# Kernel tuning notes

Measured on AMD Instinct MI355X. Metric: run time of the kernel, lower is better.

## Reference

```python
import jax, jax.numpy as jnp
import numpy as np

N_NODES = 100000
N_EDGES = 1000000
D_IN = 64
D_OUT = 64


def setup_inputs() -> dict:
    key = jax.random.key(0)
    k_feat, k_ei, k_ew, k_w, k_b = jax.random.split(key, 5)
    features = jax.random.normal(k_feat, (N_NODES, D_IN), dtype=jnp.float32)
    edge_index = jax.random.randint(k_ei, (2, N_EDGES), 0, N_NODES, dtype=jnp.int64)
    edge_weight = jax.random.uniform(k_ew, (N_EDGES,), dtype=jnp.float32)
    # nn.Linear(input_dim, output_dim): weight [out, in], bias [out]
    lim = 1.0 / np.sqrt(D_IN)
    W = jax.random.uniform(k_w, (D_OUT, D_IN), minval=-lim, maxval=lim, dtype=jnp.float32)
    b = jax.random.uniform(k_b, (D_OUT,), minval=-lim, maxval=lim, dtype=jnp.float32)
    return {"features": features, "edge_index": edge_index,
            "edge_weight": edge_weight, "W": W, "b": b}


def reference(features, edge_index, edge_weight, W, b):
    # gather source-node features and scale by edge weight: [E, F]
    messages = features[edge_index[0]] * edge_weight[:, None]
    # scatter-add into destination nodes (vectorized form of the per-column
    # scatter_add_ loop in the original): [N, F]
    aggregated = jax.ops.segment_sum(messages, edge_index[1],
                                     num_segments=features.shape[0])
    # residual + linear; dropout is identity in eval mode
    return (aggregated + features) @ W.T + b
```

## Files before the change

kernel.cpp:

```cpp
#include <hip/hip_runtime.h>

constexpr int N_NODES = 100000;
constexpr int N_EDGES = 1000000;
constexpr int D = 64;
constexpr int NTILES = (N_NODES + 1023) / 1024;


__global__ __launch_bounds__(256) void rank_k(
    const int* __restrict__ ei, int* __restrict__ cnt, int* __restrict__ rank)
{
    int e = blockIdx.x * 256 + threadIdx.x;
    if (e >= N_EDGES) return;
    rank[e] = atomicAdd(&cnt[ei[N_EDGES + e]], 1);
}

__global__ __launch_bounds__(256) void hist_k(
    const int* __restrict__ ei, int* __restrict__ hist)
{
    int e = blockIdx.x * 256 + threadIdx.x;
    if (e >= N_EDGES) return;
    atomicAdd(&hist[ei[N_EDGES + e]], 1);
}

__global__ __launch_bounds__(256) void tile_sum_k(
    const int* __restrict__ counts, int* __restrict__ tileSums)
{
    __shared__ int red[256];
    int t = threadIdx.x;
    int base = blockIdx.x * 1024 + t * 4;
    int4 c = make_int4(0, 0, 0, 0);
    if (base + 3 < N_NODES) {
        c = *reinterpret_cast<const int4*>(counts + base);
    } else {
        if (base + 0 < N_NODES) c.x = counts[base + 0];
        if (base + 1 < N_NODES) c.y = counts[base + 1];
        if (base + 2 < N_NODES) c.z = counts[base + 2];
        if (base + 3 < N_NODES) c.w = counts[base + 3];
    }
    red[t] = c.x + c.y + c.z + c.w;
    __syncthreads();
    for (int d = 128; d > 0; d >>= 1) {
        if (t < d) red[t] += red[t + d];
        __syncthreads();
    }
    if (t == 0) tileSums[blockIdx.x] = red[0];
}

__global__ __launch_bounds__(128) void tile_scan_k(
    const int* __restrict__ tileSums, int* __restrict__ tileBase)
{
    __shared__ int s[128];
    int t = threadIdx.x;
    s[t] = (t < NTILES) ? tileSums[t] : 0;
    __syncthreads();
    for (int d = 1; d < 128; d <<= 1) {
        int v = (t >= d) ? s[t - d] : 0;
        __syncthreads();
        s[t] += v;
        __syncthreads();
    }
    if (t < NTILES) tileBase[t] = t ? s[t - 1] : 0;
}

__global__ __launch_bounds__(256) void scan_apply_k(
    int* __restrict__ counts, const int* __restrict__ tileBase,
    int* __restrict__ offsets)
{
    __shared__ int tsum[256];
    int t = threadIdx.x;
    int base = blockIdx.x * 1024 + t * 4;
    int4 c = make_int4(0, 0, 0, 0);
    bool full = (base + 3 < N_NODES);
    if (full) {
        c = *reinterpret_cast<const int4*>(counts + base);
    } else {
        if (base + 0 < N_NODES) c.x = counts[base + 0];
        if (base + 1 < N_NODES) c.y = counts[base + 1];
        if (base + 2 < N_NODES) c.z = counts[base + 2];
        if (base + 3 < N_NODES) c.w = counts[base + 3];
    }
    tsum[t] = c.x + c.y + c.z + c.w;
    __syncthreads();
    for (int d = 1; d < 256; d <<= 1) {
        int v = (t >= d) ? tsum[t - d] : 0;
        __syncthreads();
        tsum[t] += v;
        __syncthreads();
    }
    int run = tileBase[blockIdx.x] + (t ? tsum[t - 1] : 0);
    int4 o = make_int4(run, run + c.x, run + c.x + c.y, run + c.x + c.y + c.z);
    if (full) {
        *reinterpret_cast<int4*>(offsets + base) = o;
        *reinterpret_cast<int4*>(counts  + base) = o;
    } else {
        if (base + 0 < N_NODES) { offsets[base + 0] = o.x; counts[base + 0] = o.x; }
        if (base + 1 < N_NODES) { offsets[base + 1] = o.y; counts[base + 1] = o.y; }
        if (base + 2 < N_NODES) { offsets[base + 2] = o.z; counts[base + 2] = o.z; }
        if (base + 3 < N_NODES) { offsets[base + 3] = o.w; counts[base + 3] = o.w; }
    }
    if (blockIdx.x == 0 && t == 0) offsets[N_NODES] = N_EDGES;
}

__global__ __launch_bounds__(256) void place_k(
    const int*   __restrict__ ei,
    const float* __restrict__ ew,
    const int*   __restrict__ rank,
    const int*   __restrict__ offsets,
    int2*        __restrict__ sorted_e)
{
    int e = blockIdx.x * 256 + threadIdx.x;
    if (e >= N_EDGES) return;
    int dst = ei[N_EDGES + e];
    int pos = offsets[dst] + rank[e];
    sorted_e[pos] = make_int2(ei[e], __float_as_int(ew[e]));
}

__global__ __launch_bounds__(256) void reorder_k(
    const int*   __restrict__ ei,
    const float* __restrict__ ew,
    int*         __restrict__ cursor,
    int2*        __restrict__ sorted_e)
{
    int e = blockIdx.x * 256 + threadIdx.x;
    if (e >= N_EDGES) return;
    int src = ei[e];
    int dst = ei[N_EDGES + e];
    int pos = atomicAdd(&cursor[dst], 1);
    sorted_e[pos] = make_int2(src, __float_as_int(ew[e]));
}

__global__ __launch_bounds__(256) void agg_gemm_k(
    const float* __restrict__ feat,
    const int2*  __restrict__ sorted_e,
    const int*   __restrict__ offsets,
    const float* __restrict__ W,
    const float* __restrict__ bias,
    float*       __restrict__ out)
{
    constexpr int PITCH = 68;
    constexpr int NPB = 16;
    __shared__ float Wl[D * PITCH];
    __shared__ float xs[NPB][D];

    int tid = threadIdx.x;
    for (int i = tid; i < D * D; i += 256)
        Wl[(i >> 6) * PITCH + (i & 63)] = W[i];

    int lane = tid & 63;
    int wv   = tid >> 6;
    int g    = lane >> 4;
    int sub  = lane & 15;

    int slot = wv * 4 + g;
    int n    = blockIdx.x * NPB + slot;
    int lo = offsets[n], hi = offsets[n + 1];
    int deg = hi - lo;

    float4 acc = *reinterpret_cast<const float4*>(feat + (size_t)n * D + sub * 4);

    const int2* ep = sorted_e + lo;
#pragma unroll 2
    for (int j = 0; j < deg; ++j) {
        int2  er = ep[j];
        float w  = __int_as_float(er.y);
        float4 f = *reinterpret_cast<const float4*>(
            feat + (size_t)er.x * D + sub * 4);
        acc.x = fmaf(f.x, w, acc.x);
        acc.y = fmaf(f.y, w, acc.y);
        acc.z = fmaf(f.z, w, acc.z);
        acc.w = fmaf(f.w, w, acc.w);
    }
    *reinterpret_cast<float4*>(&xs[slot][sub * 4]) = acc;
    __syncthreads();

    const float4* w4 = reinterpret_cast<const float4*>(&Wl[lane * PITCH]);
    const float4* x0 = reinterpret_cast<const float4*>(&xs[wv * 4 + 0][0]);
    const float4* x1 = reinterpret_cast<const float4*>(&xs[wv * 4 + 1][0]);
    const float4* x2 = reinterpret_cast<const float4*>(&xs[wv * 4 + 2][0]);
    const float4* x3 = reinterpret_cast<const float4*>(&xs[wv * 4 + 3][0]);
    float b = bias[lane];
    float a0 = b, a1 = b, a2 = b, a3 = b;
#pragma unroll
    for (int i = 0; i < 16; ++i) {
        float4 wq = w4[i];
        float4 v0 = x0[i];
        float4 v1 = x1[i];
        float4 v2 = x2[i];
        float4 v3 = x3[i];
        a0 += v0.x * wq.x + v0.y * wq.y + v0.z * wq.z + v0.w * wq.w;
        a1 += v1.x * wq.x + v1.y * wq.y + v1.z * wq.z + v1.w * wq.w;
        a2 += v2.x * wq.x + v2.y * wq.y + v2.z * wq.z + v2.w * wq.w;
        a3 += v3.x * wq.x + v3.y * wq.y + v3.z * wq.z + v3.w * wq.w;
    }
    int nb = blockIdx.x * NPB + wv * 4;
    out[(size_t)(nb + 0) * D + lane] = a0;
    out[(size_t)(nb + 1) * D + lane] = a1;
    out[(size_t)(nb + 2) * D + lane] = a2;
    out[(size_t)(nb + 3) * D + lane] = a3;
}


__global__ __launch_bounds__(256) void scatter_k(
    const float* __restrict__ feat,
    const int*   __restrict__ ei,
    const float* __restrict__ ew,
    float*       __restrict__ agg)
{
    int gid = blockIdx.x * 256 + threadIdx.x;
    int e = gid >> 4;
    if (e >= N_EDGES) return;
    int c = (gid & 15) * 4;
    int   src = ei[e];
    int   dst = ei[N_EDGES + e];
    float w   = ew[e];
    float4 f = *reinterpret_cast<const float4*>(feat + (size_t)src * D + c);
    float* a = agg + (size_t)dst * D + c;
    atomicAdd(a + 0, f.x * w);
    atomicAdd(a + 1, f.y * w);
    atomicAdd(a + 2, f.z * w);
    atomicAdd(a + 3, f.w * w);
}

__global__ __launch_bounds__(256) void gemm_k(
    const float* __restrict__ agg,
    const float* __restrict__ feat,
    const float* __restrict__ W,
    const float* __restrict__ bias,
    float*       __restrict__ out)
{
    constexpr int PITCH = 68;
    __shared__ float Wl[D * PITCH];
    __shared__ float xs[4][D];
    int tid = threadIdx.x;
    for (int i = tid; i < D * D; i += 256)
        Wl[(i >> 6) * PITCH + (i & 63)] = W[i];
    int o  = tid & 63;
    int wv = tid >> 6;
    int n  = blockIdx.x * 4 + wv;
    float b = bias[o];
    if (n < N_NODES)
        xs[wv][o] = agg[(size_t)n * D + o] + feat[(size_t)n * D + o];
    __syncthreads();
    if (n >= N_NODES) return;
    const float4* x4 = reinterpret_cast<const float4*>(&xs[wv][0]);
    const float4* w4 = reinterpret_cast<const float4*>(&Wl[o * PITCH]);
    float acc = b;
#pragma unroll
    for (int i = 0; i < 16; ++i) {
        float4 xv = x4[i];
        float4 wq = w4[i];
        acc += xv.x * wq.x + xv.y * wq.y + xv.z * wq.z + xv.w * wq.w;
    }
    out[(size_t)n * D + o] = acc;
}


extern "C" void kernel_launch(void* const* d_in, const int* in_sizes, int n_in,
                              void* d_out, int out_size, void* d_ws, size_t ws_size,
                              hipStream_t stream) {
    const float* feat = (const float*)d_in[0];
    const int*   ei   = (const int*)d_in[1];
    const float* ew   = (const float*)d_in[2];
    const float* W    = (const float*)d_in[3];
    const float* b    = (const float*)d_in[4];
    float*       out  = (float*)d_out;

    constexpr size_t NPAD       = 100352;
    constexpr size_t CNT_OFF    = 0;
    constexpr size_t OFFSET_OFF = NPAD * sizeof(int);
    constexpr size_t RANK_OFF   = 2 * NPAD * sizeof(int);
    constexpr size_t SORT1_OFF  = RANK_OFF + (size_t)N_EDGES * sizeof(int);
    constexpr size_t WS_RANK    = SORT1_OFF + (size_t)N_EDGES * sizeof(int2);
    constexpr size_t SORT2_OFF  = RANK_OFF;
    constexpr size_t WS_SORT    = SORT2_OFF + (size_t)N_EDGES * sizeof(int2);

    if (ws_size >= WS_RANK) {
        int*  cnt      = (int*)((char*)d_ws + CNT_OFF);
        int*  offsets  = (int*)((char*)d_ws + OFFSET_OFF);
        int*  rank     = (int*)((char*)d_ws + RANK_OFF);
        int2* sorted_e = (int2*)((char*)d_ws + SORT1_OFF);
        int*  tileSums = cnt + 100096;
        int*  tileBase = cnt + 100224;

        hipMemsetAsync(cnt, 0, N_NODES * sizeof(int), stream);
        rank_k     <<<(N_EDGES + 255) / 256, 256, 0, stream>>>(ei, cnt, rank);
        tile_sum_k <<<NTILES, 256, 0, stream>>>(cnt, tileSums);
        tile_scan_k<<<1, 128, 0, stream>>>(tileSums, tileBase);
        scan_apply_k<<<NTILES, 256, 0, stream>>>(cnt, tileBase, offsets);
        place_k    <<<(N_EDGES + 255) / 256, 256, 0, stream>>>(ei, ew, rank, offsets, sorted_e);
        agg_gemm_k <<<N_NODES / 16, 256, 0, stream>>>(feat, sorted_e, offsets, W, b, out);
    } else if (ws_size >= WS_SORT) {
        int*  cnt      = (int*)((char*)d_ws + CNT_OFF);
        int*  offsets  = (int*)((char*)d_ws + OFFSET_OFF);
        int2* sorted_e = (int2*)((char*)d_ws + SORT2_OFF);
        int*  tileSums = cnt + 100096;
        int*  tileBase = cnt + 100224;

        hipMemsetAsync(cnt, 0, N_NODES * sizeof(int), stream);
        hist_k     <<<(N_EDGES + 255) / 256, 256, 0, stream>>>(ei, cnt);
        tile_sum_k <<<NTILES, 256, 0, stream>>>(cnt, tileSums);
        tile_scan_k<<<1, 128, 0, stream>>>(tileSums, tileBase);
        scan_apply_k<<<NTILES, 256, 0, stream>>>(cnt, tileBase, offsets);
        reorder_k  <<<(N_EDGES + 255) / 256, 256, 0, stream>>>(ei, ew, cnt, sorted_e);
        agg_gemm_k <<<N_NODES / 16, 256, 0, stream>>>(feat, sorted_e, offsets, W, b, out);
    } else {
        const size_t agg_bytes = (size_t)N_NODES * D * sizeof(float);
        float* agg = (ws_size >= agg_bytes) ? (float*)d_ws : out;
        hipMemsetAsync(agg, 0, agg_bytes, stream);
        scatter_k<<<(N_EDGES * 16) / 256, 256, 0, stream>>>(feat, ei, ew, agg);
        gemm_k<<<(N_NODES + 3) / 4, 256, 0, stream>>>(agg, feat, W, b, out);
    }
}
```

Baseline: 203.7 us.

## Replace CSR sort with fixed-capacity per-node buckets plus overflow fixup

Builds the adjacency with fixed 32-slot buckets per destination node, filled by one atomic pass. This drops the rank, scan and place kernels. Edges beyond capacity go to an overflow list that a single-block fixup kernel applies through atomic adds of the projected message. The bucket array is large (about 25.6 MB), so the layout costs extra workspace and sparse memory traffic. Overflow edges are processed serially by one block, so skewed degree distributions would run slowly.

After: 209.8 us. 3.0% more time.

```diff
diff --git a/kernel.cpp b/kernel.cpp
--- a/kernel.cpp
+++ b/kernel.cpp
@@ -4,135 +4,36 @@
 constexpr int N_EDGES = 1000000;
 constexpr int D = 64;
 constexpr int NTILES = (N_NODES + 1023) / 1024;
-
-
-__global__ __launch_bounds__(256) void rank_k(
-    const int* __restrict__ ei, int* __restrict__ cnt, int* __restrict__ rank)
-{
-    int e = blockIdx.x * 256 + threadIdx.x;
-    if (e >= N_EDGES) return;
-    rank[e] = atomicAdd(&cnt[ei[N_EDGES + e]], 1);
-}
-
-__global__ __launch_bounds__(256) void hist_k(
-    const int* __restrict__ ei, int* __restrict__ hist)
-{
-    int e = blockIdx.x * 256 + threadIdx.x;
-    if (e >= N_EDGES) return;
-    atomicAdd(&hist[ei[N_EDGES + e]], 1);
-}
-
-__global__ __launch_bounds__(256) void tile_sum_k(
-    const int* __restrict__ counts, int* __restrict__ tileSums)
-{
-    __shared__ int red[256];
-    int t = threadIdx.x;
-    int base = blockIdx.x * 1024 + t * 4;
-    int4 c = make_int4(0, 0, 0, 0);
-    if (base + 3 < N_NODES) {
-        c = *reinterpret_cast<const int4*>(counts + base);
-    } else {
-        if (base + 0 < N_NODES) c.x = counts[base + 0];
-        if (base + 1 < N_NODES) c.y = counts[base + 1];
-        if (base + 2 < N_NODES) c.z = counts[base + 2];
-        if (base + 3 < N_NODES) c.w = counts[base + 3];
-    }
-    red[t] = c.x + c.y + c.z + c.w;
-    __syncthreads();
-    for (int d = 128; d > 0; d >>= 1) {
-        if (t < d) red[t] += red[t + d];
-        __syncthreads();
-    }
-    if (t == 0) tileSums[blockIdx.x] = red[0];
-}
-
-__global__ __launch_bounds__(128) void tile_scan_k(
-    const int* __restrict__ tileSums, int* __restrict__ tileBase)
-{
-    __shared__ int s[128];
-    int t = threadIdx.x;
-    s[t] = (t < NTILES) ? tileSums[t] : 0;
-    __syncthreads();
-    for (int d = 1; d < 128; d <<= 1) {
-        int v = (t >= d) ? s[t - d] : 0;
-        __syncthreads();
-        s[t] += v;
-        __syncthreads();
-    }
-    if (t < NTILES) tileBase[t] = t ? s[t - 1] : 0;
-}
-
-__global__ __launch_bounds__(256) void scan_apply_k(
-    int* __restrict__ counts, const int* __restrict__ tileBase,
-    int* __restrict__ offsets)
-{
-    __shared__ int tsum[256];
-    int t = threadIdx.x;
-    int base = blockIdx.x * 1024 + t * 4;
-    int4 c = make_int4(0, 0, 0, 0);
-    bool full = (base + 3 < N_NODES);
-    if (full) {
-        c = *reinterpret_cast<const int4*>(counts + base);
-    } else {
-        if (base + 0 < N_NODES) c.x = counts[base + 0];
-        if (base + 1 < N_NODES) c.y = counts[base + 1];
-        if (base + 2 < N_NODES) c.z = counts[base + 2];
-        if (base + 3 < N_NODES) c.w = counts[base + 3];
-    }
-    tsum[t] = c.x + c.y + c.z + c.w;
-    __syncthreads();
-    for (int d = 1; d < 256; d <<= 1) {
-        int v = (t >= d) ? tsum[t - d] : 0;
-        __syncthreads();
-        tsum[t] += v;
-        __syncthreads();
-    }
-    int run = tileBase[blockIdx.x] + (t ? tsum[t - 1] : 0);
-    int4 o = make_int4(run, run + c.x, run + c.x + c.y, run + c.x + c.y + c.z);
-    if (full) {
-        *reinterpret_cast<int4*>(offsets + base) = o;
-        *reinterpret_cast<int4*>(counts  + base) = o;
-    } else {
-        if (base + 0 < N_NODES) { offsets[base + 0] = o.x; counts[base + 0] = o.x; }
-        if (base + 1 < N_NODES) { offsets[base + 1] = o.y; counts[base + 1] = o.y; }
-        if (base + 2 < N_NODES) { offsets[base + 2] = o.z; counts[base + 2] = o.z; }
-        if (base + 3 < N_NODES) { offsets[base + 3] = o.w; counts[base + 3] = o.w; }
-    }
-    if (blockIdx.x == 0 && t == 0) offsets[N_NODES] = N_EDGES;
-}
-
-__global__ __launch_bounds__(256) void place_k(
+constexpr int CAP = 32;
+constexpr int OVF_CAP = 65536;
+
+
+__global__ __launch_bounds__(256) void build_k(
     const int*   __restrict__ ei,
     const float* __restrict__ ew,
-    const int*   __restrict__ rank,
-    const int*   __restrict__ offsets,
-    int2*        __restrict__ sorted_e)
-{
-    int e = blockIdx.x * 256 + threadIdx.x;
-    if (e >= N_EDGES) return;
-    int dst = ei[N_EDGES + e];
-    int pos = offsets[dst] + rank[e];
-    sorted_e[pos] = make_int2(ei[e], __float_as_int(ew[e]));
-}
-
-__global__ __launch_bounds__(256) void reorder_k(
-    const int*   __restrict__ ei,
-    const float* __restrict__ ew,
-    int*         __restrict__ cursor,
-    int2*        __restrict__ sorted_e)
+    int*         __restrict__ cnt,
+    int2*        __restrict__ buckets,
+    int*         __restrict__ ovfCount,
+    int4*        __restrict__ ovf)
 {
     int e = blockIdx.x * 256 + threadIdx.x;
     if (e >= N_EDGES) return;
     int src = ei[e];
     int dst = ei[N_EDGES + e];
-    int pos = atomicAdd(&cursor[dst], 1);
-    sorted_e[pos] = make_int2(src, __float_as_int(ew[e]));
-}
-
-__global__ __launch_bounds__(256) void agg_gemm_k(
+    int wb  = __float_as_int(ew[e]);
+    int pos = atomicAdd(&cnt[dst], 1);
+    if (pos < CAP) {
+        buckets[(size_t)dst * CAP + pos] = make_int2(src, wb);
+    } else {
+        int oi = atomicAdd(ovfCount, 1);
+        if (oi < OVF_CAP) ovf[oi] = make_int4(dst, src, wb, 0);
+    }
+}
+
+__global__ __launch_bounds__(256) void agg_gemm_bucket_k(
     const float* __restrict__ feat,
-    const int2*  __restrict__ sorted_e,
-    const int*   __restrict__ offsets,
+    const int2*  __restrict__ buckets,
+    const int*   __restrict__ cnt,
     const float* __restrict__ W,
     const float* __restrict__ bias,
     float*       __restrict__ out)
@@ -153,12 +54,12 @@
 
     int slot = wv * 4 + g;
     int n    = blockIdx.x * NPB + slot;
-    int lo = offsets[n], hi = offsets[n + 1];
-    int deg = hi - lo;
 
     float4 acc = *reinterpret_cast<const float4*>(feat + (size_t)n * D + sub * 4);
 
-    const int2* ep = sorted_e + lo;
+    int deg = cnt[n];
+    if (deg > CAP) deg = CAP;
+    const int2* ep = buckets + (size_t)n * CAP;
 #pragma unroll 2
     for (int j = 0; j < deg; ++j) {
         int2  er = ep[j];
@@ -199,6 +100,199 @@
     out[(size_t)(nb + 3) * D + lane] = a3;
 }
 
+__global__ __launch_bounds__(256) void fixup_k(
+    const float* __restrict__ feat,
+    const float* __restrict__ W,
+    const int*   __restrict__ ovfCount,
+    const int4*  __restrict__ ovf,
+    float*       __restrict__ out)
+{
+    int m = *ovfCount;
+    if (m > OVF_CAP) m = OVF_CAP;
+    for (int i = threadIdx.x + blockIdx.x * 256; i < m; i += 256) {
+        int4 r = ovf[i];
+        float w = __int_as_float(r.z);
+        for (int o = 0; o < D; ++o) {
+            float acc = 0.f;
+            for (int k = 0; k < D; ++k)
+                acc += feat[(size_t)r.y * D + k] * W[o * D + k];
+            atomicAdd(&out[(size_t)r.x * D + o], w * acc);
+        }
+    }
+}
+
+
+__global__ __launch_bounds__(256) void rank_k(
+    const int* __restrict__ ei, int* __restrict__ cnt, int* __restrict__ rank)
+{
+    int e = blockIdx.x * 256 + threadIdx.x;
+    if (e >= N_EDGES) return;
+    rank[e] = atomicAdd(&cnt[ei[N_EDGES + e]], 1);
+}
+
+__global__ __launch_bounds__(256) void tile_sum_k(
+    const int* __restrict__ counts, int* __restrict__ tileSums)
+{
+    __shared__ int red[256];
+    int t = threadIdx.x;
+    int base = blockIdx.x * 1024 + t * 4;
+    int4 c = make_int4(0, 0, 0, 0);
+    if (base + 3 < N_NODES) {
+        c = *reinterpret_cast<const int4*>(counts + base);
+    } else {
+        if (base + 0 < N_NODES) c.x = counts[base + 0];
+        if (base + 1 < N_NODES) c.y = counts[base + 1];
+        if (base + 2 < N_NODES) c.z = counts[base + 2];
+        if (base + 3 < N_NODES) c.w = counts[base + 3];
+    }
+    red[t] = c.x + c.y + c.z + c.w;
+    __syncthreads();
+    for (int d = 128; d > 0; d >>= 1) {
+        if (t < d) red[t] += red[t + d];
+        __syncthreads();
+    }
+    if (t == 0) tileSums[blockIdx.x] = red[0];
+}
+
+__global__ __launch_bounds__(128) void tile_scan_k(
+    const int* __restrict__ tileSums, int* __restrict__ tileBase)
+{
+    __shared__ int s[128];
+    int t = threadIdx.x;
+    s[t] = (t < NTILES) ? tileSums[t] : 0;
+    __syncthreads();
+    for (int d = 1; d < 128; d <<= 1) {
+        int v = (t >= d) ? s[t - d] : 0;
+        __syncthreads();
+        s[t] += v;
+        __syncthreads();
+    }
+    if (t < NTILES) tileBase[t] = t ? s[t - 1] : 0;
+}
+
+__global__ __launch_bounds__(256) void scan_apply_k(
+    int* __restrict__ counts, const int* __restrict__ tileBase,
+    int* __restrict__ offsets)
+{
+    __shared__ int tsum[256];
+    int t = threadIdx.x;
+    int base = blockIdx.x * 1024 + t * 4;
+    int4 c = make_int4(0, 0, 0, 0);
+    bool full = (base + 3 < N_NODES);
+    if (full) {
+        c = *reinterpret_cast<const int4*>(counts + base);
+    } else {
+        if (base + 0 < N_NODES) c.x = counts[base + 0];
+        if (base + 1 < N_NODES) c.y = counts[base + 1];
+        if (base + 2 < N_NODES) c.z = counts[base + 2];
+        if (base + 3 < N_NODES) c.w = counts[base + 3];
+    }
+    tsum[t] = c.x + c.y + c.z + c.w;
+    __syncthreads();
+    for (int d = 1; d < 256; d <<= 1) {
+        int v = (t >= d) ? tsum[t - d] : 0;
+        __syncthreads();
+        tsum[t] += v;
+        __syncthreads();
+    }
+    int run = tileBase[blockIdx.x] + (t ? tsum[t - 1] : 0);
+    int4 o = make_int4(run, run + c.x, run + c.x + c.y, run + c.x + c.y + c.z);
+    if (full) {
+        *reinterpret_cast<int4*>(offsets + base) = o;
+        *reinterpret_cast<int4*>(counts  + base) = o;
+    } else {
+        if (base + 0 < N_NODES) { offsets[base + 0] = o.x; counts[base + 0] = o.x; }
+        if (base + 1 < N_NODES) { offsets[base + 1] = o.y; counts[base + 1] = o.y; }
+        if (base + 2 < N_NODES) { offsets[base + 2] = o.z; counts[base + 2] = o.z; }
+        if (base + 3 < N_NODES) { offsets[base + 3] = o.w; counts[base + 3] = o.w; }
+    }
+    if (blockIdx.x == 0 && t == 0) offsets[N_NODES] = N_EDGES;
+}
+
+__global__ __launch_bounds__(256) void place_k(
+    const int*   __restrict__ ei,
+    const float* __restrict__ ew,
+    const int*   __restrict__ rank,
+    const int*   __restrict__ offsets,
+    int2*        __restrict__ sorted_e)
+{
+    int e = blockIdx.x * 256 + threadIdx.x;
+    if (e >= N_EDGES) return;
+    int dst = ei[N_EDGES + e];
+    int pos = offsets[dst] + rank[e];
+    sorted_e[pos] = make_int2(ei[e], __float_as_int(ew[e]));
+}
+
+__global__ __launch_bounds__(256) void agg_gemm_k(
+    const float* __restrict__ feat,
+    const int2*  __restrict__ sorted_e,
+    const int*   __restrict__ offsets,
+    const float* __restrict__ W,
+    const float* __restrict__ bias,
+    float*       __restrict__ out)
+{
+    constexpr int PITCH = 68;
+    constexpr int NPB = 16;
+    __shared__ float Wl[D * PITCH];
+    __shared__ float xs[NPB][D];
+
+    int tid = threadIdx.x;
+    for (int i = tid; i < D * D; i += 256)
+        Wl[(i >> 6) * PITCH + (i & 63)] = W[i];
+
+    int lane = tid & 63;
+    int wv   = tid >> 6;
+    int g    = lane >> 4;
+    int sub  = lane & 15;
+
+    int slot = wv * 4 + g;
+    int n    = blockIdx.x * NPB + slot;
+    int lo = offsets[n], hi = offsets[n + 1];
+    int deg = hi - lo;
+
+    float4 acc = *reinterpret_cast<const float4*>(feat + (size_t)n * D + sub * 4);
+
+    const int2* ep = sorted_e + lo;
+#pragma unroll 2
+    for (int j = 0; j < deg; ++j) {
+        int2  er = ep[j];
+        float w  = __int_as_float(er.y);
+        float4 f = *reinterpret_cast<const float4*>(
+            feat + (size_t)er.x * D + sub * 4);
+        acc.x = fmaf(f.x, w, acc.x);
+        acc.y = fmaf(f.y, w, acc.y);
+        acc.z = fmaf(f.z, w, acc.z);
+        acc.w = fmaf(f.w, w, acc.w);
+    }
+    *reinterpret_cast<float4*>(&xs[slot][sub * 4]) = acc;
+    __syncthreads();
+
+    const float4* w4 = reinterpret_cast<const float4*>(&Wl[lane * PITCH]);
+    const float4* x0 = reinterpret_cast<const float4*>(&xs[wv * 4 + 0][0]);
+    const float4* x1 = reinterpret_cast<const float4*>(&xs[wv * 4 + 1][0]);
+    const float4* x2 = reinterpret_cast<const float4*>(&xs[wv * 4 + 2][0]);
+    const float4* x3 = reinterpret_cast<const float4*>(&xs[wv * 4 + 3][0]);
+    float b = bias[lane];
+    float a0 = b, a1 = b, a2 = b, a3 = b;
+#pragma unroll
+    for (int i = 0; i < 16; ++i) {
+        float4 wq = w4[i];
+        float4 v0 = x0[i];
+        float4 v1 = x1[i];
+        float4 v2 = x2[i];
+        float4 v3 = x3[i];
+        a0 += v0.x * wq.x + v0.y * wq.y + v0.z * wq.z + v0.w * wq.w;
+        a1 += v1.x * wq.x + v1.y * wq.y + v1.z * wq.z + v1.w * wq.w;
+        a2 += v2.x * wq.x + v2.y * wq.y + v2.z * wq.z + v2.w * wq.w;
+        a3 += v3.x * wq.x + v3.y * wq.y + v3.z * wq.z + v3.w * wq.w;
+    }
+    int nb = blockIdx.x * NPB + wv * 4;
+    out[(size_t)(nb + 0) * D + lane] = a0;
+    out[(size_t)(nb + 1) * D + lane] = a1;
+    out[(size_t)(nb + 2) * D + lane] = a2;
+    out[(size_t)(nb + 3) * D + lane] = a3;
+}
+
 
 __global__ __launch_bounds__(256) void scatter_k(
     const float* __restrict__ feat,
@@ -265,20 +359,35 @@
     const float* b    = (const float*)d_in[4];
     float*       out  = (float*)d_out;
 
-    constexpr size_t NPAD       = 100352;
+    constexpr size_t NPAD = 100352;
+
     constexpr size_t CNT_OFF    = 0;
+    constexpr size_t BUCKET_OFF = NPAD * sizeof(int);
+    constexpr size_t OVF_OFF    = BUCKET_OFF + (size_t)N_NODES * CAP * sizeof(int2);
+    constexpr size_t WS_BUCKET  = OVF_OFF + (size_t)OVF_CAP * sizeof(int4);
+
     constexpr size_t OFFSET_OFF = NPAD * sizeof(int);
     constexpr size_t RANK_OFF   = 2 * NPAD * sizeof(int);
-    constexpr size_t SORT1_OFF  = RANK_OFF + (size_t)N_EDGES * sizeof(int);
-    constexpr size_t WS_RANK    = SORT1_OFF + (size_t)N_EDGES * sizeof(int2);
-    constexpr size_t SORT2_OFF  = RANK_OFF;
-    constexpr size_t WS_SORT    = SORT2_OFF + (size_t)N_EDGES * sizeof(int2);
-
-    if (ws_size >= WS_RANK) {
+    constexpr size_t SORT_OFF   = RANK_OFF + (size_t)N_EDGES * sizeof(int);
+    constexpr size_t WS_SORT    = SORT_OFF + (size_t)N_EDGES * sizeof(int2);
+
+    if (ws_size >= WS_BUCKET) {
+        int*  cnt      = (int*)((char*)d_ws + CNT_OFF);
+        int*  ovfCount = cnt + 100104;
+        int2* buckets  = (int2*)((char*)d_ws + BUCKET_OFF);
+        int4* ovf      = (int4*)((char*)d_ws + OVF_OFF);
+
+        hipMemsetAsync(cnt, 0, (100104 + 1) * sizeof(int), stream);
+        build_k<<<(N_EDGES + 255) / 256, 256, 0, stream>>>(
+            ei, ew, cnt, buckets, ovfCount, ovf);
+        agg_gemm_bucket_k<<<N_NODES / 16, 256, 0, stream>>>(
+            feat, buckets, cnt, W, b, out);
+        fixup_k<<<1, 256, 0, stream>>>(feat, W, ovfCount, ovf, out);
+    } else if (ws_size >= WS_SORT) {
         int*  cnt      = (int*)((char*)d_ws + CNT_OFF);
         int*  offsets  = (int*)((char*)d_ws + OFFSET_OFF);
         int*  rank     = (int*)((char*)d_ws + RANK_OFF);
-        int2* sorted_e = (int2*)((char*)d_ws + SORT1_OFF);
+        int2* sorted_e = (int2*)((char*)d_ws + SORT_OFF);
         int*  tileSums = cnt + 100096;
         int*  tileBase = cnt + 100224;
 
@@ -289,20 +398,6 @@
         scan_apply_k<<<NTILES, 256, 0, stream>>>(cnt, tileBase, offsets);
         place_k    <<<(N_EDGES + 255) / 256, 256, 0, stream>>>(ei, ew, rank, offsets, sorted_e);
         agg_gemm_k <<<N_NODES / 16, 256, 0, stream>>>(feat, sorted_e, offsets, W, b, out);
-    } else if (ws_size >= WS_SORT) {
-        int*  cnt      = (int*)((char*)d_ws + CNT_OFF);
-        int*  offsets  = (int*)((char*)d_ws + OFFSET_OFF);
-        int2* sorted_e = (int2*)((char*)d_ws + SORT2_OFF);
-        int*  tileSums = cnt + 100096;
-        int*  tileBase = cnt + 100224;
-
-        hipMemsetAsync(cnt, 0, N_NODES * sizeof(int), stream);
-        hist_k     <<<(N_EDGES + 255) / 256, 256, 0, stream>>>(ei, cnt);
-        tile_sum_k <<<NTILES, 256, 0, stream>>>(cnt, tileSums);
-        tile_scan_k<<<1, 128, 0, stream>>>(tileSums, tileBase);
-        scan_apply_k<<<NTILES, 256, 0, stream>>>(cnt, tileBase, offsets);
-        reorder_k  <<<(N_EDGES + 255) / 256, 256, 0, stream>>>(ei, ew, cnt, sorted_e);
-        agg_gemm_k <<<N_NODES / 16, 256, 0, stream>>>(feat, sorted_e, offsets, W, b, out);
     } else {
         const size_t agg_bytes = (size_t)N_NODES * D * sizeof(float);
         float* agg = (ws_size >= agg_bytes) ? (float*)d_ws : out;
```
